# Kernel optimization log

Measured on AMD Instinct MI355X. Metric: run time of the kernel, lower is better.

## Reference

```python
import jax, jax.numpy as jnp
import numpy as np

NPOINT = 2048
RADIUS = 0.1
NSAMPLE = 32


def fps(xyz, npoint):
    # Furthest point sampling, deterministic start at index 0 (matches pointnet2_utils).
    B, N, _ = xyz.shape
    dist0 = jnp.full((B, N), 1e10, dtype=xyz.dtype)
    far0 = jnp.zeros((B,), dtype=jnp.int32)

    def step(carry, _):
        dist, far = carry
        centroid = jnp.take_along_axis(xyz, far[:, None, None], axis=1)  # (B,1,3)
        d = jnp.sum((xyz - centroid) ** 2, axis=-1)                      # (B,N)
        dist = jnp.minimum(dist, d)
        new_far = jnp.argmax(dist, axis=-1).astype(jnp.int32)
        return (dist, new_far), far

    _, idx = jax.lax.scan(step, (dist0, far0), None, length=npoint)
    return idx.T  # (B, npoint)


def ball_query(xyz, new_xyz, radius, nsample):
    # For each center, indices of up to nsample points within radius (pad with first hit).
    N = xyz.shape[1]
    sqr = jnp.sum((new_xyz[:, :, None, :] - xyz[:, None, :, :]) ** 2, axis=-1)  # (B,S,N)
    cand = jnp.where(sqr <= radius * radius, jnp.arange(N, dtype=jnp.int32), N)
    cand = jnp.sort(cand, axis=-1)[:, :, :nsample]  # (B,S,K)
    first = cand[:, :, :1]
    first = jnp.where(first == N, 0, first)
    return jnp.where(cand == N, first, cand)


def batched_gather(points, idx):
    # points (B,N,C), idx (B,...) -> (B,...,C)
    return jax.vmap(lambda p, i: p[i])(points, idx)


def reference(xyz, features, W0, b0, W1, b1, W2, b2):
    # xyz: (B,N,3), features: (B,C,N)
    fps_idx = fps(xyz, NPOINT)                                  # (B,S)
    new_xyz = batched_gather(xyz, fps_idx)                      # (B,S,3)
    idx = ball_query(xyz, new_xyz, RADIUS, NSAMPLE)             # (B,S,K)

    grouped_xyz = batched_gather(xyz, idx) - new_xyz[:, :, None, :]   # (B,S,K,3) relative coords
    grouped_feat = batched_gather(features.transpose(0, 2, 1), idx)   # (B,S,K,C)
    grouped = jnp.concatenate([grouped_xyz, grouped_feat], axis=-1)   # (B,S,K,C+3)
    x = grouped.transpose(0, 3, 1, 2)                                 # (B,C+3,S,K)

    # SharedMLP: 1x1 conv2d + ReLU stack
    x = jax.nn.relu(jnp.einsum('oi,bisk->bosk', W0, x) + b0[None, :, None, None])
    x = jax.nn.relu(jnp.einsum('oi,bisk->bosk', W1, x) + b1[None, :, None, None])
    x = jax.nn.relu(jnp.einsum('oi,bisk->bosk', W2, x) + b2[None, :, None, None])

    new_features = jnp.max(x, axis=-1)  # max-pool over nsample -> (B,128,S)
    return new_xyz, new_features


def setup_inputs() -> dict:
    key = jax.random.key(0)
    ks = jax.random.split(key, 8)
    B, N, C = 4, 8192, 64
    s = 0.05  # keep activations in a sane range through 3 relu layers
    return {
        'xyz': jax.random.uniform(ks[0], (B, N, 3), dtype=jnp.float32),
        'features': jax.random.normal(ks[1], (B, C, N), dtype=jnp.float32),
        'W0': jax.random.normal(ks[2], (64, 67), dtype=jnp.float32) * s,
        'b0': jax.random.normal(ks[3], (64,), dtype=jnp.float32) * s,
        'W1': jax.random.normal(ks[4], (64, 64), dtype=jnp.float32) * s,
        'b1': jax.random.normal(ks[5], (64,), dtype=jnp.float32) * s,
        'W2': jax.random.normal(ks[6], (128, 64), dtype=jnp.float32) * s,
        'b2': jax.random.normal(ks[7], (128,), dtype=jnp.float32) * s,
    }
```

## Files before the change

kernel.cpp:

```cpp
#include <hip/hip_runtime.h>

#define NB 4
#define NPTS 8192
#define NPOINT 2048
#define NSAMPLE 32
#define CF 64
#define CIN 67
#define G 8

typedef float f32x2 __attribute__((ext_vector_type(2)));
typedef unsigned long long u64;

__device__ __forceinline__ f32x2 pk_add(f32x2 a, f32x2 b) {
  f32x2 d;
  asm("v_pk_add_f32 %0, %1, %2" : "=v"(d) : "v"(a), "v"(b));
  return d;
}
__device__ __forceinline__ f32x2 pk_mul(f32x2 a, f32x2 b) {
  f32x2 d;
  asm("v_pk_mul_f32 %0, %1, %2" : "=v"(d) : "v"(a), "v"(b));
  return d;
}

template <int CTRL, int RM>
__device__ __forceinline__ int dppi(int v) {
  return __builtin_amdgcn_update_dpp(0, v, CTRL, RM, 0xf, true);
}
__device__ __forceinline__ double kmax(double a, double b) { return fmax(a, b); }
__device__ __forceinline__ double mkkey(unsigned hi, unsigned lo) {
  return __longlong_as_double(((long long)hi << 32) | lo);
}
template <int CTRL, int RM>
__device__ __forceinline__ double kstep_d(double k) {
  long long bb = __double_as_longlong(k);
  unsigned lo = (unsigned)bb, hi = (unsigned)(bb >> 32);
  unsigned olo = (unsigned)dppi<CTRL, RM>((int)lo);
  unsigned ohi = (unsigned)dppi<CTRL, RM>((int)hi);
  double o = __longlong_as_double(((long long)ohi << 32) | olo);
  return fmax(k, o);
}
__device__ __forceinline__ double wave_max_key_d(double key) {
  key = kstep_d<0x111, 0xf>(key);
  key = kstep_d<0x112, 0xf>(key);
  key = kstep_d<0x114, 0xf>(key);
  key = kstep_d<0x118, 0xf>(key);
  key = kstep_d<0x142, 0xa>(key);
  key = kstep_d<0x143, 0xc>(key);
  return key;
}
__device__ __forceinline__ unsigned wave_scan_incl(unsigned v) {
  v += (unsigned)__builtin_amdgcn_update_dpp(0, (int)v, 0x111, 0xf, 0xf, true);
  v += (unsigned)__builtin_amdgcn_update_dpp(0, (int)v, 0x112, 0xf, 0xf, true);
  v += (unsigned)__builtin_amdgcn_update_dpp(0, (int)v, 0x114, 0xf, 0xf, true);
  v += (unsigned)__builtin_amdgcn_update_dpp(0, (int)v, 0x118, 0xf, 0xf, true);
  v += (unsigned)__builtin_amdgcn_update_dpp(0, (int)v, 0x142, 0xa, 0xf, true);
  v += (unsigned)__builtin_amdgcn_update_dpp(0, (int)v, 0x143, 0xc, 0xf, true);
  return v;
}

__device__ __forceinline__ int cell16(float x) {
  int c = (int)(x * 16.0f);
  return c > 15 ? 15 : (c < 0 ? 0 : c);
}
__device__ __forceinline__ unsigned morton12(int ix, int iy, int iz) {
  unsigned m = 0;
#pragma unroll
  for (int k = 0; k < 4; ++k) {
    m |= ((unsigned)((ix >> k) & 1) << (3 * k + 2)) |
         ((unsigned)((iy >> k) & 1) << (3 * k + 1)) |
         ((unsigned)((iz >> k) & 1) << (3 * k + 0));
  }
  return m;
}

__global__ __launch_bounds__(512) void fps_kernel(const float* __restrict__ xyz,
                                                  float* __restrict__ new_xyz) {
  const int b = blockIdx.x;
  const int tid = threadIdx.x;
  const int lane = tid & 63;
  const int wid = tid >> 6;
  __shared__ float sx[NPTS], sy[NPTS], sz[NPTS];
  __shared__ unsigned short sidx16[NPTS];
  __shared__ unsigned offs[4096];
  __shared__ unsigned wsum[8];
  __shared__ int farhist[NPOINT];
  __shared__ __align__(16) double skey[2][8];

  const float* xb = xyz + (size_t)b * NPTS * 3;
  for (int i = tid; i < NPTS; i += 512) {
    sx[i] = xb[3 * i + 0];
    sy[i] = xb[3 * i + 1];
    sz[i] = xb[3 * i + 2];
  }
  for (int i = tid; i < 4096; i += 512) offs[i] = 0;
  __syncthreads();
  for (int r = 0; r < 16; ++r) {
    int i = tid + r * 512;
    atomicAdd(&offs[morton12(cell16(sx[i]), cell16(sy[i]), cell16(sz[i]))], 1u);
  }
  __syncthreads();
  unsigned loc[8];
  unsigned s = 0;
#pragma unroll
  for (int q = 0; q < 8; ++q) {
    loc[q] = s;
    s += offs[tid * 8 + q];
  }
  unsigned inc = wave_scan_incl(s);
  if (lane == 63) wsum[wid] = inc;
  __syncthreads();
  unsigned pre = 0;
#pragma unroll
  for (int w = 0; w < 8; ++w) pre += (w < wid) ? wsum[w] : 0u;
  unsigned excl = pre + inc - s;
  __syncthreads();
#pragma unroll
  for (int q = 0; q < 8; ++q) offs[tid * 8 + q] = excl + loc[q];
  __syncthreads();
  for (int r = 0; r < 16; ++r) {
    int i = tid + r * 512;
    unsigned m = morton12(cell16(sx[i]), cell16(sy[i]), cell16(sz[i]));
    unsigned pos = atomicAdd(&offs[m], 1u);
    sidx16[pos] = (unsigned short)i;
  }
  __syncthreads();

  f32x2 px[8], py[8], pz[8];
  float dist[16];
  unsigned noid[16];
  float blx = 1e30f, bhx = -1e30f, bly = 1e30f, bhy = -1e30f,
        blz = 1e30f, bhz = -1e30f;
#pragma unroll
  for (int j = 0; j < 8; ++j) {
    unsigned i0 = sidx16[tid * 16 + 2 * j], i1 = sidx16[tid * 16 + 2 * j + 1];
    noid[2 * j] = ~i0; noid[2 * j + 1] = ~i1;
    float x0 = sx[i0], x1 = sx[i1];
    float y0 = sy[i0], y1 = sy[i1];
    float z0 = sz[i0], z1 = sz[i1];
    px[j].x = x0; px[j].y = x1;
    py[j].x = y0; py[j].y = y1;
    pz[j].x = z0; pz[j].y = z1;
    blx = fminf(blx, fminf(x0, x1)); bhx = fmaxf(bhx, fmaxf(x0, x1));
    bly = fminf(bly, fminf(y0, y1)); bhy = fmaxf(bhy, fmaxf(y0, y1));
    blz = fminf(blz, fminf(z0, z1)); bhz = fmaxf(bhz, fmaxf(z0, z1));
    dist[2 * j] = 1e10f; dist[2 * j + 1] = 1e10f;
  }
  float gmaxd = 1e30f;
  double gkey = 0.0;
  int far = 0;
  for (int it = 0; it < NPOINT; ++it) {
    if (tid == 0) farhist[it] = far;
    const float cx = sx[far], cy = sy[far], cz = sz[far];
    float gx = fmaxf(fmaxf(blx - cx, cx - bhx), 0.f);
    float gy = fmaxf(fmaxf(bly - cy, cy - bhy), 0.f);
    float gz = fmaxf(fmaxf(blz - cz, cz - bhz), 0.f);
    float mind2 = gx * gx + gy * gy + gz * gz;
    if (mind2 * 0.999f < gmaxd) {
      f32x2 ncx, ncy, ncz;
      ncx.x = -cx; ncx.y = -cx;
      ncy.x = -cy; ncy.y = -cy;
      ncz.x = -cz; ncz.y = -cz;
      double kk[16];
#pragma unroll
      for (int j = 0; j < 8; ++j) {
        f32x2 dx = pk_add(px[j], ncx);
        f32x2 dy = pk_add(py[j], ncy);
        f32x2 dz = pk_add(pz[j], ncz);
        f32x2 xx = pk_mul(dx, dx);
        f32x2 yy = pk_mul(dy, dy);
        f32x2 dd = pk_add(pk_add(xx, yy), pk_mul(dz, dz));
        float n0 = fminf(dist[2 * j], dd.x);
        float n1 = fminf(dist[2 * j + 1], dd.y);
        dist[2 * j] = n0; dist[2 * j + 1] = n1;
        kk[2 * j] = mkkey(__float_as_uint(n0), noid[2 * j]);
        kk[2 * j + 1] = mkkey(__float_as_uint(n1), noid[2 * j + 1]);
      }
#pragma unroll
      for (int st = 1; st < 16; st <<= 1)
#pragma unroll
        for (int j = 0; j < 16; j += 2 * st) kk[j] = kmax(kk[j], kk[j + st]);
      gkey = kk[0];
      gmaxd = __uint_as_float((unsigned)((u64)__double_as_longlong(kk[0]) >> 32));
    }
    double key = wave_max_key_d(gkey);
    const int p = it & 1;
    if (lane == 63) skey[p][wid] = key;
    __syncthreads();
    const double2* kp = (const double2*)&skey[p][0];
    double2 a0 = kp[0], a1 = kp[1], a2 = kp[2], a3 = kp[3];
    double q0 = kmax(a0.x, a0.y), q1 = kmax(a1.x, a1.y);
    double q2 = kmax(a2.x, a2.y), q3 = kmax(a3.x, a3.y);
    double best = kmax(kmax(q0, q1), kmax(q2, q3));
    far = (int)~(unsigned)(u64)__double_as_longlong(best);
  }
  __syncthreads();
  for (int t = tid; t < NPOINT; t += 512) {
    int f = farhist[t];
    float* o = new_xyz + ((size_t)b * NPOINT + t) * 3;
    o[0] = sx[f]; o[1] = sy[f]; o[2] = sz[f];
  }
}

__global__ __launch_bounds__(256) void tr_kernel(const float* __restrict__ f,
                                                 float* __restrict__ ft) {
  int idx = blockIdx.x * 256 + threadIdx.x;
  int c = idx & 63;
  int i = (idx >> 6) & (NPTS - 1);
  int b = idx >> 19;
  ft[idx] = f[((size_t)(b * CF + c)) * NPTS + i];
}

__global__ __launch_bounds__(256) void bq_kernel(const float* __restrict__ xyz,
                                                 const float* __restrict__ new_xyz,
                                                 int* __restrict__ idxbuf) {
  const int lane = threadIdx.x & 63;
  const int gw = (blockIdx.x * 256 + threadIdx.x) >> 6;
  const int b = gw >> 11;
  const int j = gw & 2047;
  const float* xb = xyz + (size_t)b * NPTS * 3;
  const float* c = new_xyz + ((size_t)b * NPOINT + j) * 3;
  const float cx = c[0], cy = c[1], cz = c[2];
  int* out = idxbuf + ((size_t)b * NPOINT + j) * NSAMPLE;
  const float r2 = 0.01f;
  int found = 0, first = 0;
  for (int base = 0; base < NPTS && found < NSAMPLE; base += 64) {
    const int i = base + lane;
    float dx = xb[3 * i + 0] - cx, dy = xb[3 * i + 1] - cy, dz = xb[3 * i + 2] - cz;
    float d = __fadd_rn(__fadd_rn(__fmul_rn(dx, dx), __fmul_rn(dy, dy)),
                        __fmul_rn(dz, dz));
    bool in = (d <= r2);
    unsigned long long mask = __ballot(in);
    if (mask) {
      if (found == 0) first = base + (__ffsll(mask) - 1);
      int slot = found + __popcll(mask & ((1ull << lane) - 1ull));
      if (in && slot < NSAMPLE) out[slot] = i;
      found += (int)__popcll(mask);
    }
  }
  for (int s = found + lane; s < NSAMPLE; s += 64) out[s] = first;
}

__global__ __launch_bounds__(256) void mlp_kernel(const float* __restrict__ xyz,
                                                  const float* __restrict__ ft,
                                                  const float* __restrict__ feat,
                                                  const int* __restrict__ idxbuf,
                                                  const float* __restrict__ new_xyz,
                                                  const float* __restrict__ W0,
                                                  const float* __restrict__ b0,
                                                  const float* __restrict__ W1,
                                                  const float* __restrict__ b1,
                                                  const float* __restrict__ W2,
                                                  const float* __restrict__ b2,
                                                  float* __restrict__ out_nf,
                                                  int use_ft) {
  __shared__ __align__(16) float Ws0[CIN * 64];
  __shared__ __align__(16) float Ws1[64 * 64];
  __shared__ __align__(16) float Ws2[64 * 128];
  __shared__ float bs0[64], bs1[64], bs2[128];
  __shared__ __align__(16) float X0[CIN * 32];
  __shared__ __align__(16) float X1[64 * 32];
  const int tid = threadIdx.x;
  const int k = tid & 31;
  const int og = tid >> 5;
  for (int t = tid; t < 64 * CIN; t += 256) {
    int o = t / CIN, c = t - o * CIN;
    Ws0[c * 64 + o] = W0[t];
  }
  for (int t = tid; t < 64 * 64; t += 256) Ws1[(t & 63) * 64 + (t >> 6)] = W1[t];
  for (int t = tid; t < 128 * 64; t += 256) Ws2[(t & 63) * 128 + (t >> 6)] = W2[t];
  if (tid < 64) { bs0[tid] = b0[tid]; bs1[tid] = b1[tid]; }
  if (tid < 128) bs2[tid] = b2[tid];
  __syncthreads();

  for (int g = 0; g < G; ++g) {
    const int cj = blockIdx.x * G + g;
    const int b = cj >> 11;
    const int j = cj & 2047;
    const int ni = idxbuf[cj * NSAMPLE + k];
    if (og == 0) {
      const float* ctr = new_xyz + (size_t)cj * 3;
      const float* pp = xyz + ((size_t)b * NPTS + ni) * 3;
      X0[0 * 32 + k] = pp[0] - ctr[0];
      X0[1 * 32 + k] = pp[1] - ctr[1];
      X0[2 * 32 + k] = pp[2] - ctr[2];
    }
    const int cbase = 3 + og * 8;
    if (use_ft) {
      const float4* fr = (const float4*)(ft + ((size_t)b * NPTS + ni) * CF + og * 8);
      float4 f0 = fr[0], f1 = fr[1];
      X0[(cbase + 0) * 32 + k] = f0.x; X0[(cbase + 1) * 32 + k] = f0.y;
      X0[(cbase + 2) * 32 + k] = f0.z; X0[(cbase + 3) * 32 + k] = f0.w;
      X0[(cbase + 4) * 32 + k] = f1.x; X0[(cbase + 5) * 32 + k] = f1.y;
      X0[(cbase + 6) * 32 + k] = f1.z; X0[(cbase + 7) * 32 + k] = f1.w;
    } else {
      const float* fb = feat + (size_t)b * CF * NPTS + ni;
#pragma unroll
      for (int q = 0; q < 8; ++q)
        X0[(cbase + q) * 32 + k] = fb[(size_t)(og * 8 + q) * NPTS];
    }
    __syncthreads();

    float acc[8];
#pragma unroll
    for (int i = 0; i < 8; ++i) acc[i] = bs0[og * 8 + i];
    for (int c = 0; c < CIN; ++c) {
      float xv = X0[c * 32 + k];
      const float4* wr = (const float4*)&Ws0[c * 64 + og * 8];
      float4 w0 = wr[0], w1 = wr[1];
      acc[0] = fmaf(w0.x, xv, acc[0]); acc[1] = fmaf(w0.y, xv, acc[1]);
      acc[2] = fmaf(w0.z, xv, acc[2]); acc[3] = fmaf(w0.w, xv, acc[3]);
      acc[4] = fmaf(w1.x, xv, acc[4]); acc[5] = fmaf(w1.y, xv, acc[5]);
      acc[6] = fmaf(w1.z, xv, acc[6]); acc[7] = fmaf(w1.w, xv, acc[7]);
    }
#pragma unroll
    for (int i = 0; i < 8; ++i) X1[(og * 8 + i) * 32 + k] = fmaxf(acc[i], 0.f);
    __syncthreads();

    float a1[8];
#pragma unroll
    for (int i = 0; i < 8; ++i) a1[i] = bs1[og * 8 + i];
    for (int c = 0; c < 64; ++c) {
      float xv = X1[c * 32 + k];
      const float4* wr = (const float4*)&Ws1[c * 64 + og * 8];
      float4 w0 = wr[0], w1 = wr[1];
      a1[0] = fmaf(w0.x, xv, a1[0]); a1[1] = fmaf(w0.y, xv, a1[1]);
      a1[2] = fmaf(w0.z, xv, a1[2]); a1[3] = fmaf(w0.w, xv, a1[3]);
      a1[4] = fmaf(w1.x, xv, a1[4]); a1[5] = fmaf(w1.y, xv, a1[5]);
      a1[6] = fmaf(w1.z, xv, a1[6]); a1[7] = fmaf(w1.w, xv, a1[7]);
    }
#pragma unroll
    for (int i = 0; i < 8; ++i) X0[(og * 8 + i) * 32 + k] = fmaxf(a1[i], 0.f);
    __syncthreads();

    float a2[16];
#pragma unroll
    for (int i = 0; i < 16; ++i) a2[i] = bs2[og * 16 + i];
    for (int c = 0; c < 64; ++c) {
      float xv = X0[c * 32 + k];
      const float4* wr = (const float4*)&Ws2[c * 128 + og * 16];
      float4 w0 = wr[0], w1 = wr[1], w2 = wr[2], w3 = wr[3];
      a2[0]  = fmaf(w0.x, xv, a2[0]);  a2[1]  = fmaf(w0.y, xv, a2[1]);
      a2[2]  = fmaf(w0.z, xv, a2[2]);  a2[3]  = fmaf(w0.w, xv, a2[3]);
      a2[4]  = fmaf(w1.x, xv, a2[4]);  a2[5]  = fmaf(w1.y, xv, a2[5]);
      a2[6]  = fmaf(w1.z, xv, a2[6]);  a2[7]  = fmaf(w1.w, xv, a2[7]);
      a2[8]  = fmaf(w2.x, xv, a2[8]);  a2[9]  = fmaf(w2.y, xv, a2[9]);
      a2[10] = fmaf(w2.z, xv, a2[10]); a2[11] = fmaf(w2.w, xv, a2[11]);
      a2[12] = fmaf(w3.x, xv, a2[12]); a2[13] = fmaf(w3.y, xv, a2[13]);
      a2[14] = fmaf(w3.z, xv, a2[14]); a2[15] = fmaf(w3.w, xv, a2[15]);
    }
#pragma unroll
    for (int i = 0; i < 16; ++i) {
      float v = fmaxf(a2[i], 0.f);
#pragma unroll
      for (int m = 1; m < 32; m <<= 1) v = fmaxf(v, __shfl_xor(v, m));
      a2[i] = v;
    }
    if (k == 0) {
#pragma unroll
      for (int i = 0; i < 16; ++i)
        out_nf[((size_t)b * 128 + og * 16 + i) * NPOINT + j] = a2[i];
    }
    __syncthreads();
  }
}

extern "C" void kernel_launch(void* const* d_in, const int* in_sizes, int n_in,
                              void* d_out, int out_size, void* d_ws, size_t ws_size,
                              hipStream_t stream) {
  (void)in_sizes; (void)n_in; (void)out_size;
  const float* xyz  = (const float*)d_in[0];
  const float* feat = (const float*)d_in[1];
  const float* W0   = (const float*)d_in[2];
  const float* b0   = (const float*)d_in[3];
  const float* W1   = (const float*)d_in[4];
  const float* b1   = (const float*)d_in[5];
  const float* W2   = (const float*)d_in[6];
  const float* b2   = (const float*)d_in[7];
  float* new_xyz = (float*)d_out;
  float* out_nf  = (float*)d_out + (size_t)NB * NPOINT * 3;

  int* idxbuf = (int*)d_ws;
  size_t idx_bytes = (size_t)NB * NPOINT * NSAMPLE * sizeof(int);
  float* ft = (float*)((char*)d_ws + idx_bytes);
  size_t need = idx_bytes + (size_t)NB * NPTS * CF * sizeof(float);
  int use_ft = (ws_size >= need) ? 1 : 0;

  fps_kernel<<<NB, 512, 0, stream>>>(xyz, new_xyz);
  if (use_ft) tr_kernel<<<(NB * NPTS * CF) / 256, 256, 0, stream>>>(feat, ft);
  bq_kernel<<<(NB * NPOINT) / 4, 256, 0, stream>>>(xyz, new_xyz, idxbuf);
  mlp_kernel<<<(NB * NPOINT) / G, 256, 0, stream>>>(xyz, ft, feat, idxbuf, new_xyz,
                                                    W0, b0, W1, b1, W2, b2,
                                                    out_nf, use_ft);
}
```

Before: 1.989 ms.

## Run FPS loop in a single wavefront with LDS-resident distances and Morton-sorted coordinates

The furthest point sampling loop now runs on one 64-lane wavefront instead of eight waves. This removes the per-iteration __syncthreads and the cross-wave key reduction. Coordinates are scattered into Morton order in shared memory, and distances live in LDS. Each lane owns eight 16-point subgroups, each with a bounding box, so only dirty subgroups are recomputed. The cost is that a single wave processes all 8192 points per dirty iteration with LDS traffic, which may lose throughput compared with spreading the work across 512 threads.

```diff
diff --git a/kernel.cpp b/kernel.cpp
--- a/kernel.cpp
+++ b/kernel.cpp
@@ -8,19 +8,7 @@
 #define CIN 67
 #define G 8
 
-typedef float f32x2 __attribute__((ext_vector_type(2)));
 typedef unsigned long long u64;
-
-__device__ __forceinline__ f32x2 pk_add(f32x2 a, f32x2 b) {
-  f32x2 d;
-  asm("v_pk_add_f32 %0, %1, %2" : "=v"(d) : "v"(a), "v"(b));
-  return d;
-}
-__device__ __forceinline__ f32x2 pk_mul(f32x2 a, f32x2 b) {
-  f32x2 d;
-  asm("v_pk_mul_f32 %0, %1, %2" : "=v"(d) : "v"(a), "v"(b));
-  return d;
-}
 
 template <int CTRL, int RM>
 __device__ __forceinline__ int dppi(int v) {
@@ -79,24 +67,21 @@
   const int tid = threadIdx.x;
   const int lane = tid & 63;
   const int wid = tid >> 6;
-  __shared__ float sx[NPTS], sy[NPTS], sz[NPTS];
-  __shared__ unsigned short sidx16[NPTS];
-  __shared__ unsigned offs[4096];
+  __shared__ __align__(16) float sxs[NPTS], sys[NPTS], szs[NPTS];
+  __shared__ __align__(16) float sdist[NPTS];
+  __shared__ __align__(16) unsigned short sidx16[NPTS];
   __shared__ unsigned wsum[8];
   __shared__ int farhist[NPOINT];
-  __shared__ __align__(16) double skey[2][8];
+  __shared__ int spos0s;
+  unsigned* offs = (unsigned*)sdist;
 
   const float* xb = xyz + (size_t)b * NPTS * 3;
-  for (int i = tid; i < NPTS; i += 512) {
-    sx[i] = xb[3 * i + 0];
-    sy[i] = xb[3 * i + 1];
-    sz[i] = xb[3 * i + 2];
-  }
   for (int i = tid; i < 4096; i += 512) offs[i] = 0;
   __syncthreads();
   for (int r = 0; r < 16; ++r) {
     int i = tid + r * 512;
-    atomicAdd(&offs[morton12(cell16(sx[i]), cell16(sy[i]), cell16(sz[i]))], 1u);
+    float x = xb[3 * i + 0], y = xb[3 * i + 1], z = xb[3 * i + 2];
+    atomicAdd(&offs[morton12(cell16(x), cell16(y), cell16(z))], 1u);
   }
   __syncthreads();
   unsigned loc[8];
@@ -119,85 +104,143 @@
   __syncthreads();
   for (int r = 0; r < 16; ++r) {
     int i = tid + r * 512;
-    unsigned m = morton12(cell16(sx[i]), cell16(sy[i]), cell16(sz[i]));
+    float x = xb[3 * i + 0], y = xb[3 * i + 1], z = xb[3 * i + 2];
+    unsigned m = morton12(cell16(x), cell16(y), cell16(z));
     unsigned pos = atomicAdd(&offs[m], 1u);
+    sxs[pos] = x; sys[pos] = y; szs[pos] = z;
     sidx16[pos] = (unsigned short)i;
-  }
-  __syncthreads();
-
-  f32x2 px[8], py[8], pz[8];
-  float dist[16];
-  unsigned noid[16];
-  float blx = 1e30f, bhx = -1e30f, bly = 1e30f, bhy = -1e30f,
-        blz = 1e30f, bhz = -1e30f;
-#pragma unroll
-  for (int j = 0; j < 8; ++j) {
-    unsigned i0 = sidx16[tid * 16 + 2 * j], i1 = sidx16[tid * 16 + 2 * j + 1];
-    noid[2 * j] = ~i0; noid[2 * j + 1] = ~i1;
-    float x0 = sx[i0], x1 = sx[i1];
-    float y0 = sy[i0], y1 = sy[i1];
-    float z0 = sz[i0], z1 = sz[i1];
-    px[j].x = x0; px[j].y = x1;
-    py[j].x = y0; py[j].y = y1;
-    pz[j].x = z0; pz[j].y = z1;
-    blx = fminf(blx, fminf(x0, x1)); bhx = fmaxf(bhx, fmaxf(x0, x1));
-    bly = fminf(bly, fminf(y0, y1)); bhy = fmaxf(bhy, fmaxf(y0, y1));
-    blz = fminf(blz, fminf(z0, z1)); bhz = fmaxf(bhz, fmaxf(z0, z1));
-    dist[2 * j] = 1e10f; dist[2 * j + 1] = 1e10f;
-  }
-  float gmaxd = 1e30f;
-  double gkey = 0.0;
-  int far = 0;
-  for (int it = 0; it < NPOINT; ++it) {
-    if (tid == 0) farhist[it] = far;
-    const float cx = sx[far], cy = sy[far], cz = sz[far];
-    float gx = fmaxf(fmaxf(blx - cx, cx - bhx), 0.f);
-    float gy = fmaxf(fmaxf(bly - cy, cy - bhy), 0.f);
-    float gz = fmaxf(fmaxf(blz - cz, cz - bhz), 0.f);
-    float mind2 = gx * gx + gy * gy + gz * gz;
-    if (mind2 * 0.999f < gmaxd) {
-      f32x2 ncx, ncy, ncz;
-      ncx.x = -cx; ncx.y = -cx;
-      ncy.x = -cy; ncy.y = -cy;
-      ncz.x = -cz; ncz.y = -cz;
-      double kk[16];
-#pragma unroll
-      for (int j = 0; j < 8; ++j) {
-        f32x2 dx = pk_add(px[j], ncx);
-        f32x2 dy = pk_add(py[j], ncy);
-        f32x2 dz = pk_add(pz[j], ncz);
-        f32x2 xx = pk_mul(dx, dx);
-        f32x2 yy = pk_mul(dy, dy);
-        f32x2 dd = pk_add(pk_add(xx, yy), pk_mul(dz, dz));
-        float n0 = fminf(dist[2 * j], dd.x);
-        float n1 = fminf(dist[2 * j + 1], dd.y);
-        dist[2 * j] = n0; dist[2 * j + 1] = n1;
-        kk[2 * j] = mkkey(__float_as_uint(n0), noid[2 * j]);
-        kk[2 * j + 1] = mkkey(__float_as_uint(n1), noid[2 * j + 1]);
+    if (i == 0) spos0s = (int)pos;
+  }
+  __syncthreads();
+  for (int i = tid; i < NPTS; i += 512) sdist[i] = 1e10f;
+  __syncthreads();
+
+  if (wid == 0) {
+    float blx[8], bhx[8], bly[8], bhy[8], blz[8], bhz[8];
+    double ck[8];
+    float gmd[8];
+#pragma unroll
+    for (int sg = 0; sg < 8; ++sg) {
+      const int base = sg * 1024 + lane * 16;
+      const float4* x4 = (const float4*)&sxs[base];
+      const float4* y4 = (const float4*)&sys[base];
+      const float4* z4 = (const float4*)&szs[base];
+      float lx = 1e30f, hx = -1e30f, ly = 1e30f, hy = -1e30f,
+            lz = 1e30f, hz = -1e30f;
+#pragma unroll
+      for (int q = 0; q < 4; ++q) {
+        float4 xv = x4[q], yv = y4[q], zv = z4[q];
+        lx = fminf(lx, fminf(fminf(xv.x, xv.y), fminf(xv.z, xv.w)));
+        hx = fmaxf(hx, fmaxf(fmaxf(xv.x, xv.y), fmaxf(xv.z, xv.w)));
+        ly = fminf(ly, fminf(fminf(yv.x, yv.y), fminf(yv.z, yv.w)));
+        hy = fmaxf(hy, fmaxf(fmaxf(yv.x, yv.y), fmaxf(yv.z, yv.w)));
+        lz = fminf(lz, fminf(fminf(zv.x, zv.y), fminf(zv.z, zv.w)));
+        hz = fmaxf(hz, fmaxf(fmaxf(zv.x, zv.y), fmaxf(zv.z, zv.w)));
       }
-#pragma unroll
-      for (int st = 1; st < 16; st <<= 1)
-#pragma unroll
-        for (int j = 0; j < 16; j += 2 * st) kk[j] = kmax(kk[j], kk[j + st]);
-      gkey = kk[0];
-      gmaxd = __uint_as_float((unsigned)((u64)__double_as_longlong(kk[0]) >> 32));
-    }
-    double key = wave_max_key_d(gkey);
-    const int p = it & 1;
-    if (lane == 63) skey[p][wid] = key;
-    __syncthreads();
-    const double2* kp = (const double2*)&skey[p][0];
-    double2 a0 = kp[0], a1 = kp[1], a2 = kp[2], a3 = kp[3];
-    double q0 = kmax(a0.x, a0.y), q1 = kmax(a1.x, a1.y);
-    double q2 = kmax(a2.x, a2.y), q3 = kmax(a3.x, a3.y);
-    double best = kmax(kmax(q0, q1), kmax(q2, q3));
-    far = (int)~(unsigned)(u64)__double_as_longlong(best);
+      blx[sg] = lx; bhx[sg] = hx; bly[sg] = ly; bhy[sg] = hy;
+      blz[sg] = lz; bhz[sg] = hz;
+      ck[sg] = 0.0;
+      gmd[sg] = 1e30f;
+    }
+    int far = spos0s;
+    for (int it = 0; it < NPOINT; ++it) {
+      if (lane == 0) farhist[it] = far;
+      const float cx = sxs[far], cy = sys[far], cz = szs[far];
+#pragma unroll
+      for (int sg = 0; sg < 8; ++sg) {
+        float gx = fmaxf(fmaxf(blx[sg] - cx, cx - bhx[sg]), 0.f);
+        float gy = fmaxf(fmaxf(bly[sg] - cy, cy - bhy[sg]), 0.f);
+        float gz = fmaxf(fmaxf(blz[sg] - cz, cz - bhz[sg]), 0.f);
+        float mind2 = gx * gx + gy * gy + gz * gz;
+        bool dirty = mind2 * 0.999f < gmd[sg];
+        if (__ballot(dirty)) {
+          if (dirty) {
+            const int base = sg * 1024 + lane * 16;
+            const float4* x4 = (const float4*)&sxs[base];
+            const float4* y4 = (const float4*)&sys[base];
+            const float4* z4 = (const float4*)&szs[base];
+            float4* d4 = (float4*)&sdist[base];
+            const uint4* i4 = (const uint4*)&sidx16[base];
+            uint4 ia = i4[0], ib = i4[1];
+            unsigned nk[16];
+            nk[0]  = ((8191u - (ia.x & 0xffffu)) << 13) | (unsigned)(base + 0);
+            nk[1]  = ((8191u - (ia.x >> 16))     << 13) | (unsigned)(base + 1);
+            nk[2]  = ((8191u - (ia.y & 0xffffu)) << 13) | (unsigned)(base + 2);
+            nk[3]  = ((8191u - (ia.y >> 16))     << 13) | (unsigned)(base + 3);
+            nk[4]  = ((8191u - (ia.z & 0xffffu)) << 13) | (unsigned)(base + 4);
+            nk[5]  = ((8191u - (ia.z >> 16))     << 13) | (unsigned)(base + 5);
+            nk[6]  = ((8191u - (ia.w & 0xffffu)) << 13) | (unsigned)(base + 6);
+            nk[7]  = ((8191u - (ia.w >> 16))     << 13) | (unsigned)(base + 7);
+            nk[8]  = ((8191u - (ib.x & 0xffffu)) << 13) | (unsigned)(base + 8);
+            nk[9]  = ((8191u - (ib.x >> 16))     << 13) | (unsigned)(base + 9);
+            nk[10] = ((8191u - (ib.y & 0xffffu)) << 13) | (unsigned)(base + 10);
+            nk[11] = ((8191u - (ib.y >> 16))     << 13) | (unsigned)(base + 11);
+            nk[12] = ((8191u - (ib.z & 0xffffu)) << 13) | (unsigned)(base + 12);
+            nk[13] = ((8191u - (ib.z >> 16))     << 13) | (unsigned)(base + 13);
+            nk[14] = ((8191u - (ib.w & 0xffffu)) << 13) | (unsigned)(base + 14);
+            nk[15] = ((8191u - (ib.w >> 16))     << 13) | (unsigned)(base + 15);
+            double kk[16];
+#pragma unroll
+            for (int q = 0; q < 4; ++q) {
+              float4 xv = x4[q], yv = y4[q], zv = z4[q], dv = d4[q];
+              {
+                float dx = __fsub_rn(xv.x, cx), dy = __fsub_rn(yv.x, cy),
+                      dz = __fsub_rn(zv.x, cz);
+                float d = __fadd_rn(__fadd_rn(__fmul_rn(dx, dx), __fmul_rn(dy, dy)),
+                                    __fmul_rn(dz, dz));
+                dv.x = fminf(dv.x, d);
+                kk[q * 4 + 0] = mkkey(__float_as_uint(dv.x), nk[q * 4 + 0]);
+              }
+              {
+                float dx = __fsub_rn(xv.y, cx), dy = __fsub_rn(yv.y, cy),
+                      dz = __fsub_rn(zv.y, cz);
+                float d = __fadd_rn(__fadd_rn(__fmul_rn(dx, dx), __fmul_rn(dy, dy)),
+                                    __fmul_rn(dz, dz));
+                dv.y = fminf(dv.y, d);
+                kk[q * 4 + 1] = mkkey(__float_as_uint(dv.y), nk[q * 4 + 1]);
+              }
+              {
+                float dx = __fsub_rn(xv.z, cx), dy = __fsub_rn(yv.z, cy),
+                      dz = __fsub_rn(zv.z, cz);
+                float d = __fadd_rn(__fadd_rn(__fmul_rn(dx, dx), __fmul_rn(dy, dy)),
+                                    __fmul_rn(dz, dz));
+                dv.z = fminf(dv.z, d);
+                kk[q * 4 + 2] = mkkey(__float_as_uint(dv.z), nk[q * 4 + 2]);
+              }
+              {
+                float dx = __fsub_rn(xv.w, cx), dy = __fsub_rn(yv.w, cy),
+                      dz = __fsub_rn(zv.w, cz);
+                float d = __fadd_rn(__fadd_rn(__fmul_rn(dx, dx), __fmul_rn(dy, dy)),
+                                    __fmul_rn(dz, dz));
+                dv.w = fminf(dv.w, d);
+                kk[q * 4 + 3] = mkkey(__float_as_uint(dv.w), nk[q * 4 + 3]);
+              }
+              d4[q] = dv;
+            }
+#pragma unroll
+            for (int st = 1; st < 16; st <<= 1)
+#pragma unroll
+              for (int j = 0; j < 16; j += 2 * st) kk[j] = kmax(kk[j], kk[j + st]);
+            ck[sg] = kk[0];
+            gmd[sg] = __uint_as_float(
+                (unsigned)((u64)__double_as_longlong(kk[0]) >> 32));
+          }
+        }
+      }
+      double m0 = kmax(ck[0], ck[1]), m1 = kmax(ck[2], ck[3]);
+      double m2 = kmax(ck[4], ck[5]), m3 = kmax(ck[6], ck[7]);
+      double lk = kmax(kmax(m0, m1), kmax(m2, m3));
+      double wk = wave_max_key_d(lk);
+      unsigned lo63 = (unsigned)__builtin_amdgcn_readlane(
+          (int)(unsigned)(u64)__double_as_longlong(wk), 63);
+      far = (int)(lo63 & 8191u);
+    }
   }
   __syncthreads();
   for (int t = tid; t < NPOINT; t += 512) {
     int f = farhist[t];
     float* o = new_xyz + ((size_t)b * NPOINT + t) * 3;
-    o[0] = sx[f]; o[1] = sy[f]; o[2] = sz[f];
+    o[0] = sxs[f]; o[1] = sys[f]; o[2] = szs[f];
   }
 }
 
```

After: 4.572 ms. 2.3x slower.
